# Kernel tuning notes

Measured on AMD Instinct MI355X. Metric: run time of the kernel, lower is better.

## Reference

```python
import jax, jax.numpy as jnp
import numpy as np

N, E, F_IN, H, H2, G, C = 30000, 480000, 1280, 512, 256, 64, 10


def _linear_init(key, fan_in, fan_out):
    k1, k2 = jax.random.split(key)
    s = 1.0 / np.sqrt(fan_in)
    W = jax.random.uniform(k1, (fan_in, fan_out), jnp.float32, -s, s)
    b = jax.random.uniform(k2, (fan_out,), jnp.float32, -s, s)
    return W, b


def setup_inputs() -> dict:
    key = jax.random.key(0)
    ks = jax.random.split(key, 6)
    x = jax.random.normal(ks[0], (N, F_IN), jnp.float32)
    edge_index = jax.random.randint(ks[1], (2, E), 0, N, dtype=jnp.int32).astype(jnp.int64)
    batch = jnp.sort(jax.random.randint(ks[2], (N,), 0, G, dtype=jnp.int32)).astype(jnp.int64)
    W1, b1 = _linear_init(ks[3], F_IN, H)
    beta2 = jnp.ones((), jnp.float32)  # AGNNConv beta init = 1.0 (trainable in prop2)
    W2, b2 = _linear_init(ks[4], H, H2)
    W3, b3 = _linear_init(ks[5], 2 * H2, C)
    return {"x": x, "edge_index": edge_index, "batch": batch,
            "W1": W1, "b1": b1, "beta2": beta2,
            "W2": W2, "b2": b2, "W3": W3, "b3": b3}


def _agnn(x, src, dst, beta, n):
    # L2 normalize (PyG F.normalize: clamp norm at 1e-12)
    norm = jnp.maximum(jnp.linalg.norm(x, axis=-1, keepdims=True), 1e-12)
    xn = x / norm
    # per-edge cosine similarity attention logits
    alpha = beta * jnp.sum(xn[src] * xn[dst], axis=-1)  # [E']
    # softmax over incoming edges of each destination node
    amax = jax.ops.segment_max(alpha, dst, num_segments=n)
    ex = jnp.exp(alpha - amax[dst])
    denom = jax.ops.segment_sum(ex, dst, num_segments=n)
    w = ex / denom[dst]
    # weighted scatter-add of raw source features
    return jax.ops.segment_sum(w[:, None] * x[src], dst, num_segments=n)


def reference(x, edge_index, batch, W1, b1, beta2, W2, b2, W3, b3):
    n = x.shape[0]
    h = jax.nn.relu(x @ W1 + b1)  # [N, 512]
    # AGNNConv adds self-loops by default
    loops = jnp.arange(n, dtype=edge_index.dtype)
    src = jnp.concatenate([edge_index[0], loops])
    dst = jnp.concatenate([edge_index[1], loops])
    h = _agnn(h, src, dst, jnp.float32(1.0), n)  # prop1: fixed beta=1
    h = _agnn(h, src, dst, beta2, n)             # prop2: learned beta
    h = jax.nn.relu(h @ W2 + b2)  # [N, 256]
    # global max / mean pool per graph
    gmx = jax.ops.segment_max(h, batch, num_segments=G)
    cnt = jnp.maximum(jax.ops.segment_sum(jnp.ones((n,), h.dtype), batch, num_segments=G), 1.0)
    gav = jax.ops.segment_sum(h, batch, num_segments=G) / cnt[:, None]
    return jnp.concatenate([gmx, gav], axis=1) @ W3 + b3  # [G, C]
```

## Files before the change

kernel.cpp:

```cpp
#include <hip/hip_runtime.h>
#include <hip/hip_bf16.h>
#include <cstdint>


typedef __attribute__((ext_vector_type(8))) short bf16x8;
typedef __attribute__((ext_vector_type(4))) float f32x4;
typedef __attribute__((ext_vector_type(8))) unsigned short ushort8;
typedef __attribute__((ext_vector_type(4))) unsigned short ushort4v;
typedef __attribute__((ext_vector_type(4))) unsigned int uint4v;

__device__ inline unsigned short f2bf(float f) {
    unsigned int u = __float_as_uint(f);
    u += 0x7FFFu + ((u >> 16) & 1u);
    return (unsigned short)(u >> 16);
}

__device__ __forceinline__ float bf2f(unsigned short u) {
    return __uint_as_float(((unsigned int)u) << 16);
}

__device__ __forceinline__ unsigned int cvtpk(float lo, float hi) {
    unsigned int r;
    asm("v_cvt_pk_bf16_f32 %0, %1, %2" : "=v"(r) : "v"(lo), "v"(hi));
    return r;
}

__device__ __forceinline__ void gload_lds16(const void* g, void* l) {
    __builtin_amdgcn_global_load_lds(
        (const __attribute__((address_space(1))) void*)g,
        (__attribute__((address_space(3))) void*)l, 16, 0, 0);
}

__global__ __launch_bounds__(256) void k_transpose_bf16(
    const float* __restrict__ W, unsigned short* __restrict__ Wt, int K, int N) {
    __shared__ unsigned short t[32][33];
    int k0 = blockIdx.x * 32, n0 = blockIdx.y * 32;
    int tr = threadIdx.x >> 3;
    int tc = (threadIdx.x & 7) * 4;
    float4 v = *(const float4*)(W + (long)(k0 + tr) * N + n0 + tc);
    t[tr][tc + 0] = f2bf(v.x); t[tr][tc + 1] = f2bf(v.y);
    t[tr][tc + 2] = f2bf(v.z); t[tr][tc + 3] = f2bf(v.w);
    __syncthreads();
    ushort4v o = { t[tc + 0][tr], t[tc + 1][tr], t[tc + 2][tr], t[tc + 3][tr] };
    *(ushort4v*)(Wt + (long)(n0 + tr) * K + k0 + tc) = o;
}

template <int K, int N, int WGPB, bool AF32, bool OUTBF16>
__global__ __launch_bounds__(256, WGPB) void k_gemm_bias_relu(
    const void* __restrict__ Av, const unsigned short* __restrict__ Bt,
    const float* __restrict__ bias, void* __restrict__ Cv, int M) {
    constexpr int NF = N / 32;
    __shared__ unsigned short As[2][64 * 32];
    __shared__ unsigned short Bs[2][N * 32];
    int tid = threadIdx.x;
    int w = tid >> 6, l = tid & 63;
    int wm = w >> 1, wn = w & 1;
    int mBase = blockIdx.x * 64;

    const float* Af = (const float*)Av;
    const unsigned short* Ab = (const unsigned short*)Av;

    int arow = tid >> 2;
    int aslot = (tid & 3) ^ ((arow >> 1) & 3);
    long aRowG = mBase + arow; if (aRowG >= M) aRowG = M - 1;
    const float* aptr = AF32 ? (Af + aRowG * K + (tid & 3) * 8) : nullptr;

    auto stageB = [&](int b, int k0) {
#pragma unroll
        for (int o = 0; o < N / 64; ++o) {
            int rbase = (o * 4 + w) * 16;
            int row = rbase + (l >> 2);
            int gsrc = (l & 3) ^ ((row >> 1) & 3);
            gload_lds16(Bt + (long)row * K + k0 + gsrc * 8, &Bs[b][rbase * 32]);
        }
    };
    auto stageAbf = [&](int b, int k0) {
        int rbase = w * 16;
        int row = rbase + (l >> 2);
        int gsrc = (l & 3) ^ ((row >> 1) & 3);
        long gr = mBase + row; if (gr >= M) gr = M - 1;
        gload_lds16(Ab + gr * K + k0 + gsrc * 8, &As[b][rbase * 32]);
    };

    f32x4 acc[2][NF] = {};
    constexpr int NSTEP = K / 32;

    stageB(0, 0);
    if constexpr (AF32) {
        float4 f0 = *(const float4*)(aptr);
        float4 f1 = *(const float4*)(aptr + 4);
        uint4v p = { cvtpk(f0.x, f0.y), cvtpk(f0.z, f0.w),
                     cvtpk(f1.x, f1.y), cvtpk(f1.z, f1.w) };
        *(uint4v*)(&As[0][arow * 32 + aslot * 8]) = p;
    } else {
        stageAbf(0, 0);
    }
    __syncthreads();

    int s = 0;
    for (int step = 0; step < NSTEP; ++step, s ^= 1) {
        int nk = (step + 1) * 32;
        float4 f0, f1;
        if (nk < K) {
            stageB(s ^ 1, nk);
            if constexpr (AF32) {
                f0 = *(const float4*)(aptr + nk);
                f1 = *(const float4*)(aptr + nk + 4);
            } else {
                stageAbf(s ^ 1, nk);
            }
        }
        bf16x8 af[2];
#pragma unroll
        for (int m = 0; m < 2; ++m) {
            int ra = wm * 32 + m * 16 + (l & 15);
            int g = (l >> 4) ^ ((ra >> 1) & 3);
            af[m] = *(const bf16x8*)(&As[s][ra * 32 + g * 8]);
        }
#pragma unroll
        for (int n = 0; n < NF; ++n) {
            int rb = wn * (N / 2) + n * 16 + (l & 15);
            int g = (l >> 4) ^ ((rb >> 1) & 3);
            bf16x8 bfr = *(const bf16x8*)(&Bs[s][rb * 32 + g * 8]);
#pragma unroll
            for (int m = 0; m < 2; ++m)
                acc[m][n] = __builtin_amdgcn_mfma_f32_16x16x32_bf16(
                    af[m], bfr, acc[m][n], 0, 0, 0);
        }
        if constexpr (AF32) {
            if (nk < K) {
                uint4v p = { cvtpk(f0.x, f0.y), cvtpk(f0.z, f0.w),
                             cvtpk(f1.x, f1.y), cvtpk(f1.z, f1.w) };
                *(uint4v*)(&As[s ^ 1][arow * 32 + aslot * 8]) = p;
            }
        }
        __syncthreads();
    }

#pragma unroll
    for (int m = 0; m < 2; ++m) {
        int row = mBase + wm * 32 + m * 16 + (l >> 4) * 4;
#pragma unroll
        for (int n = 0; n < NF; ++n) {
            int colg = wn * (N / 2) + n * 16 + (l & 15);
            float bv = bias[colg];
#pragma unroll
            for (int r = 0; r < 4; ++r) {
                if (row + r < M) {
                    float v = fmaxf(acc[m][n][r] + bv, 0.f);
                    if constexpr (OUTBF16)
                        ((unsigned short*)Cv)[(long)(row + r) * N + colg] = f2bf(v);
                    else
                        ((float*)Cv)[(long)(row + r) * N + colg] = v;
                }
            }
        }
    }
}

__global__ void k_csr_init(int* __restrict__ cnt, int* __restrict__ fill, int n) {
    int i = blockIdx.x * blockDim.x + threadIdx.x;
    if (i < n) { cnt[i] = 1; fill[i] = 0; }
}

__global__ void k_csr_count(const int* __restrict__ ei, int* __restrict__ cnt, int E) {
    int e = blockIdx.x * blockDim.x + threadIdx.x;
    if (e < E) atomicAdd(&cnt[ei[E + e]], 1);
}

__global__ __launch_bounds__(1024) void k_scan1(const int* __restrict__ cnt,
                                                int* __restrict__ rowp,
                                                int* __restrict__ bsum, int n) {
    __shared__ int wsum[16];
    int b = blockIdx.x, t = threadIdx.x, lane = t & 63, w = t >> 6;
    int i = b * 1024 + t;
    int v = (i < n) ? cnt[i] : 0;
    int x = v;
#pragma unroll
    for (int off = 1; off < 64; off <<= 1) {
        int y = __shfl_up(x, off, 64);
        if (lane >= off) x += y;
    }
    if (lane == 63) wsum[w] = x;
    __syncthreads();
    if (t < 16) {
        int s = wsum[t];
#pragma unroll
        for (int off = 1; off < 16; off <<= 1) {
            int y = __shfl_up(s, off, 64);
            if (t >= off) s += y;
        }
        wsum[t] = s;
    }
    __syncthreads();
    int wo = w ? wsum[w - 1] : 0;
    if (i < n) rowp[i] = wo + x - v;
    if (t == 0) bsum[b] = wsum[15];
}

__global__ __launch_bounds__(64) void k_scan2(int* __restrict__ bsum, int nb) {
    int lane = threadIdx.x;
    int v = (lane < nb) ? bsum[lane] : 0;
    int x = v;
#pragma unroll
    for (int off = 1; off < 64; off <<= 1) {
        int y = __shfl_up(x, off, 64);
        if (lane >= off) x += y;
    }
    int total = __shfl(x, nb - 1, 64);
    if (lane < nb) bsum[lane] = x - v;
    if (lane == 0) bsum[nb] = total;
}

__global__ __launch_bounds__(1024) void k_scan3(const int* __restrict__ bsum,
                                                int* __restrict__ rowp, int n, int nb) {
    int i = blockIdx.x * 1024 + threadIdx.x;
    if (i < n) rowp[i] += bsum[i >> 10];
    else if (i == n) rowp[n] = bsum[nb];
}

__global__ void k_csr_fill(const int* __restrict__ ei, const int* __restrict__ rowp,
                           int* __restrict__ fill, int* __restrict__ col, int E, int n) {
    int idx = blockIdx.x * blockDim.x + threadIdx.x;
    if (idx < E) {
        int d = ei[E + idx];
        int s = ei[idx];
        int pos = atomicAdd(&fill[d], 1);
        col[rowp[d] + pos] = s;
    } else if (idx < E + n) {
        int nd = idx - E;
        int pos = atomicAdd(&fill[nd], 1);
        col[rowp[nd] + pos] = nd;
    }
}

__global__ __launch_bounds__(256) void k_norm_bf16(const unsigned short* __restrict__ h,
                                                   float* __restrict__ invn, int n) {
    int row = blockIdx.x * 4 + (threadIdx.x >> 6);
    int lane = threadIdx.x & 63;
    if (row >= n) return;
    ushort8 v = *(const ushort8*)(h + (long)row * 512 + lane * 8);
    float s = 0.f;
#pragma unroll
    for (int e = 0; e < 8; ++e) { float f = bf2f(v[e]); s += f * f; }
#pragma unroll
    for (int off = 32; off; off >>= 1) s += __shfl_xor(s, off, 64);
    if (lane == 0) invn[row] = 1.f / fmaxf(sqrtf(s), 1e-12f);
}

__global__ __launch_bounds__(256) void k_agnn(
    const unsigned short* __restrict__ h, const float* __restrict__ invn,
    const int* __restrict__ rowp, const int* __restrict__ col,
    const float* __restrict__ beta_ptr, unsigned short* __restrict__ out,
    float* __restrict__ invn_out, int nNodes) {
    int dst = blockIdx.x * 4 + (threadIdx.x >> 6);
    int lane = threadIdx.x & 63;
    if (dst >= nNodes) return;
    float beta = beta_ptr ? beta_ptr[0] : 1.0f;
    ushort8 hdv = *(const ushort8*)(h + (long)dst * 512 + lane * 8);
    float hd[8];
#pragma unroll
    for (int e = 0; e < 8; ++e) hd[e] = bf2f(hdv[e]);
    float coef = beta * invn[dst];
    int s0 = rowp[dst], s1 = rowp[dst + 1];

    float m = -1e30f, ssum = 0.f;
    float acc[8] = {0.f, 0.f, 0.f, 0.f, 0.f, 0.f, 0.f, 0.f};

    for (int base = s0; base < s1; base += 64) {
        int cnt = min(s1 - base, 64);
        int gi = base + lane; if (gi >= s1) gi = s1 - 1;
        int idxl = col[gi];
        float vinl = invn[idxl];
        int src0 = __shfl(idxl, 0, 64);
        ushort8 nxt = *(const ushort8*)(h + (long)src0 * 512 + lane * 8);
        for (int j = 0; j < cnt; ++j) {
            ushort8 cur = nxt;
            if (j + 1 < cnt) {
                int sn = __shfl(idxl, j + 1, 64);
                nxt = *(const ushort8*)(h + (long)sn * 512 + lane * 8);
            }
            float a[8];
#pragma unroll
            for (int e = 0; e < 8; ++e) a[e] = bf2f(cur[e]);
            float p = a[0] * hd[0] + a[1] * hd[1] + a[2] * hd[2] + a[3] * hd[3] +
                      a[4] * hd[4] + a[5] * hd[5] + a[6] * hd[6] + a[7] * hd[7];
#pragma unroll
            for (int off = 32; off; off >>= 1) p += __shfl_xor(p, off, 64);
            float alpha = coef * __shfl(vinl, j, 64) * p;
            if (alpha > m) {
                float sc = __expf(m - alpha);
                ssum *= sc;
#pragma unroll
                for (int e = 0; e < 8; ++e) acc[e] *= sc;
                m = alpha;
            }
            float wgt = __expf(alpha - m);
            ssum += wgt;
#pragma unroll
            for (int e = 0; e < 8; ++e) acc[e] += wgt * a[e];
        }
    }
    float inv_s = 1.f / ssum;
#pragma unroll
    for (int e = 0; e < 8; ++e) acc[e] *= inv_s;

    uint4v o = { cvtpk(acc[0], acc[1]), cvtpk(acc[2], acc[3]),
                 cvtpk(acc[4], acc[5]), cvtpk(acc[6], acc[7]) };
    *(uint4v*)(out + (long)dst * 512 + lane * 8) = o;

    if (invn_out) {
        float s = 0.f;
#pragma unroll
        for (int e = 0; e < 8; ++e) s += acc[e] * acc[e];
#pragma unroll
        for (int off = 32; off; off >>= 1) s += __shfl_xor(s, off, 64);
        if (lane == 0) invn_out[dst] = 1.f / fmaxf(sqrtf(s), 1e-12f);
    }
}

__global__ void k_bounds(const int* __restrict__ batch, int* __restrict__ starts,
                         int n, int G) {
    int g = blockIdx.x * blockDim.x + threadIdx.x;
    if (g > G) return;
    int lo = 0, hi = n;
    while (lo < hi) {
        int mid = (lo + hi) >> 1;
        if (batch[mid] < g) lo = mid + 1; else hi = mid;
    }
    starts[g] = lo;
}

__global__ __launch_bounds__(256) void k_pool(const float* __restrict__ h3,
                                              const int* __restrict__ starts,
                                              float* __restrict__ pooled) {
    int g = blockIdx.x;
    int t = threadIdx.x;
    int s = starts[g], e = starts[g + 1];
    float mx = -3.402823466e38f, sm = 0.f;
    int r = s;
    for (; r + 4 <= e; r += 4) {
        float v0 = h3[(long)(r + 0) * 256 + t];
        float v1 = h3[(long)(r + 1) * 256 + t];
        float v2 = h3[(long)(r + 2) * 256 + t];
        float v3 = h3[(long)(r + 3) * 256 + t];
        mx = fmaxf(mx, fmaxf(fmaxf(v0, v1), fmaxf(v2, v3)));
        sm += (v0 + v1) + (v2 + v3);
    }
    for (; r < e; ++r) {
        float v = h3[(long)r * 256 + t];
        mx = fmaxf(mx, v); sm += v;
    }
    float cnt = fmaxf((float)(e - s), 1.f);
    pooled[g * 512 + t] = mx;
    pooled[g * 512 + 256 + t] = sm / cnt;
}

__global__ __launch_bounds__(64) void k_final(const float* __restrict__ pooled,
                                              const float* __restrict__ W3,
                                              const float* __restrict__ b3,
                                              float* __restrict__ out, int C) {
    int g = blockIdx.x;
    int lane = threadIdx.x;
    for (int c = 0; c < C; c++) {
        float p = 0.f;
        for (int k = lane; k < 512; k += 64) p += pooled[g * 512 + k] * W3[k * C + c];
#pragma unroll
        for (int off = 32; off; off >>= 1) p += __shfl_xor(p, off, 64);
        if (lane == 0) out[g * C + c] = p + b3[c];
    }
}

extern "C" void kernel_launch(void* const* d_in, const int* in_sizes, int n_in,
                              void* d_out, int out_size, void* d_ws, size_t ws_size,
                              hipStream_t stream) {
    const float* x     = (const float*)d_in[0];
    const int*   ei    = (const int*)d_in[1];
    const int*   batch = (const int*)d_in[2];
    const float* W1    = (const float*)d_in[3];
    const float* b1    = (const float*)d_in[4];
    const float* beta2 = (const float*)d_in[5];
    const float* W2    = (const float*)d_in[6];
    const float* b2    = (const float*)d_in[7];
    const float* W3    = (const float*)d_in[8];
    const float* b3    = (const float*)d_in[9];
    float* out = (float*)d_out;

    const int N = in_sizes[2];
    const int E = in_sizes[1] / 2;
    const int F_IN = in_sizes[0] / N;
    const int H = in_sizes[4];
    const int H2 = in_sizes[7];
    const int C = in_sizes[9];
    const int G = out_size / C;

    char* ws = (char*)d_ws;
    unsigned short* H1B = (unsigned short*)(ws + 0);
    unsigned short* HPB = (unsigned short*)(ws + 31000000L);
    unsigned short* H2B = (unsigned short*)(ws + 62000000L);
    float*          H3  = (float*)(ws + 0);
    unsigned short* W1T = (unsigned short*)(ws + 93000000L);
    unsigned short* W2T = (unsigned short*)(ws + 94500000L);
    float* INVN_A = (float*)(ws + 95000000L);
    float* INVN_B = (float*)(ws + 95200000L);
    int*   CNT    = (int*)(ws + 95400000L);
    int*   FILL   = (int*)(ws + 95600000L);
    int*   ROWP   = (int*)(ws + 95800000L);
    int*   COL    = (int*)(ws + 96000000L);
    int*   BSUM   = (int*)(ws + 98100000L);
    int*   START  = (int*)(ws + 98110000L);
    float* POOLED = (float*)(ws + 98120000L);

    { dim3 g1(F_IN / 32, H / 32); k_transpose_bf16<<<g1, 256, 0, stream>>>(W1, W1T, F_IN, H); }
    { dim3 g2(H / 32, H2 / 32);   k_transpose_bf16<<<g2, 256, 0, stream>>>(W2, W2T, H, H2); }

    int nb = (N + 1023) / 1024;
    k_csr_init<<<(N + 255) / 256, 256, 0, stream>>>(CNT, FILL, N);
    k_csr_count<<<(E + 255) / 256, 256, 0, stream>>>(ei, CNT, E);
    k_scan1<<<nb, 1024, 0, stream>>>(CNT, ROWP, BSUM, N);
    k_scan2<<<1, 64, 0, stream>>>(BSUM, nb);
    k_scan3<<<(N + 1 + 1023) / 1024, 1024, 0, stream>>>(BSUM, ROWP, N, nb);
    k_csr_fill<<<(E + N + 255) / 256, 256, 0, stream>>>(ei, ROWP, FILL, COL, E, N);

    k_gemm_bias_relu<1280, 512, 2, true, true>
        <<<(N + 63) / 64, 256, 0, stream>>>(x, W1T, b1, H1B, N);

    k_norm_bf16<<<(N + 3) / 4, 256, 0, stream>>>(H1B, INVN_A, N);
    k_agnn<<<(N + 3) / 4, 256, 0, stream>>>(H1B, INVN_A, ROWP, COL, nullptr, HPB, INVN_B, N);

    k_agnn<<<(N + 3) / 4, 256, 0, stream>>>(HPB, INVN_B, ROWP, COL, beta2, H2B, nullptr, N);

    k_gemm_bias_relu<512, 256, 3, false, false>
        <<<(N + 63) / 64, 256, 0, stream>>>(H2B, W2T, b2, H3, N);

    k_bounds<<<1, 128, 0, stream>>>(batch, START, N, G);
    k_pool<<<G, 256, 0, stream>>>(H3, START, POOLED);
    k_final<<<G, 64, 0, stream>>>(POOLED, W3, b3, out, C);
}
```

Measured before the change: 395.1 us.

## Retile GEMMs to 128x256 blocks and use DPP wave reductions in AGNN

Both bias+ReLU GEMMs move to 512-thread blocks that compute a 128-row by 256-column tile, with a second grid dimension splitting the 512-wide output of the first GEMM. Each wave now holds a 64x64 accumulator, which raises MFMA work per LDS fragment load and improves operand reuse, at the cost of more registers per thread and fewer blocks. Separately, the butterfly `__shfl_xor` wave reductions in the norm and AGNN kernels are replaced by a DPP sequence followed by a readlane, and the index and norm broadcasts now use readlane. This cuts LDS-routed shuffle traffic in the per-edge inner loop.

```diff
diff --git a/kernel.cpp b/kernel.cpp
--- a/kernel.cpp
+++ b/kernel.cpp
@@ -29,6 +29,23 @@
     __builtin_amdgcn_global_load_lds(
         (const __attribute__((address_space(1))) void*)g,
         (__attribute__((address_space(3))) void*)l, 16, 0, 0);
+}
+
+__device__ __forceinline__ float wave_sum_dpp(float p) {
+    int t;
+    t = __builtin_amdgcn_update_dpp(0, __float_as_int(p), 0xB1, 0xf, 0xf, true);
+    p += __int_as_float(t);
+    t = __builtin_amdgcn_update_dpp(0, __float_as_int(p), 0x4E, 0xf, 0xf, true);
+    p += __int_as_float(t);
+    t = __builtin_amdgcn_update_dpp(0, __float_as_int(p), 0x141, 0xf, 0xf, true);
+    p += __int_as_float(t);
+    t = __builtin_amdgcn_update_dpp(0, __float_as_int(p), 0x140, 0xf, 0xf, true);
+    p += __int_as_float(t);
+    t = __builtin_amdgcn_update_dpp(0, __float_as_int(p), 0x142, 0xf, 0xf, true);
+    p += __int_as_float(t);
+    t = __builtin_amdgcn_update_dpp(0, __float_as_int(p), 0x143, 0xf, 0xf, true);
+    p += __int_as_float(t);
+    return __int_as_float(__builtin_amdgcn_readlane(__float_as_int(p), 63));
 }
 
 __global__ __launch_bounds__(256) void k_transpose_bf16(
@@ -45,17 +62,17 @@
     *(ushort4v*)(Wt + (long)(n0 + tr) * K + k0 + tc) = o;
 }
 
-template <int K, int N, int WGPB, bool AF32, bool OUTBF16>
-__global__ __launch_bounds__(256, WGPB) void k_gemm_bias_relu(
+template <int K, int BN, int NOUT, bool AF32, bool OUTBF16>
+__global__ __launch_bounds__(512, 4) void k_gemm_bias_relu(
     const void* __restrict__ Av, const unsigned short* __restrict__ Bt,
     const float* __restrict__ bias, void* __restrict__ Cv, int M) {
-    constexpr int NF = N / 32;
-    __shared__ unsigned short As[2][64 * 32];
-    __shared__ unsigned short Bs[2][N * 32];
+    __shared__ unsigned short As[2][128 * 32];
+    __shared__ unsigned short Bs[2][BN * 32];
     int tid = threadIdx.x;
     int w = tid >> 6, l = tid & 63;
-    int wm = w >> 1, wn = w & 1;
-    int mBase = blockIdx.x * 64;
+    int wm = w >> 2, wn = w & 3;
+    int mBase = blockIdx.x * 128;
+    int nBase = blockIdx.y * BN;
 
     const float* Af = (const float*)Av;
     const unsigned short* Ab = (const unsigned short*)Av;
@@ -67,11 +84,12 @@
 
     auto stageB = [&](int b, int k0) {
 #pragma unroll
-        for (int o = 0; o < N / 64; ++o) {
-            int rbase = (o * 4 + w) * 16;
+        for (int o = 0; o < BN / 128; ++o) {
+            int rbase = (w * (BN / 128) + o) * 16;
             int row = rbase + (l >> 2);
             int gsrc = (l & 3) ^ ((row >> 1) & 3);
-            gload_lds16(Bt + (long)row * K + k0 + gsrc * 8, &Bs[b][rbase * 32]);
+            gload_lds16(Bt + (long)(nBase + row) * K + k0 + gsrc * 8,
+                        &Bs[b][rbase * 32]);
         }
     };
     auto stageAbf = [&](int b, int k0) {
@@ -82,7 +100,7 @@
         gload_lds16(Ab + gr * K + k0 + gsrc * 8, &As[b][rbase * 32]);
     };
 
-    f32x4 acc[2][NF] = {};
+    f32x4 acc[4][4] = {};
     constexpr int NSTEP = K / 32;
 
     stageB(0, 0);
@@ -110,20 +128,20 @@
                 stageAbf(s ^ 1, nk);
             }
         }
-        bf16x8 af[2];
-#pragma unroll
-        for (int m = 0; m < 2; ++m) {
-            int ra = wm * 32 + m * 16 + (l & 15);
+        bf16x8 af[4];
+#pragma unroll
+        for (int m = 0; m < 4; ++m) {
+            int ra = wm * 64 + m * 16 + (l & 15);
             int g = (l >> 4) ^ ((ra >> 1) & 3);
             af[m] = *(const bf16x8*)(&As[s][ra * 32 + g * 8]);
         }
 #pragma unroll
-        for (int n = 0; n < NF; ++n) {
-            int rb = wn * (N / 2) + n * 16 + (l & 15);
+        for (int n = 0; n < 4; ++n) {
+            int rb = wn * 64 + n * 16 + (l & 15);
             int g = (l >> 4) ^ ((rb >> 1) & 3);
             bf16x8 bfr = *(const bf16x8*)(&Bs[s][rb * 32 + g * 8]);
 #pragma unroll
-            for (int m = 0; m < 2; ++m)
+            for (int m = 0; m < 4; ++m)
                 acc[m][n] = __builtin_amdgcn_mfma_f32_16x16x32_bf16(
                     af[m], bfr, acc[m][n], 0, 0, 0);
         }
@@ -138,20 +156,20 @@
     }
 
 #pragma unroll
-    for (int m = 0; m < 2; ++m) {
-        int row = mBase + wm * 32 + m * 16 + (l >> 4) * 4;
-#pragma unroll
-        for (int n = 0; n < NF; ++n) {
-            int colg = wn * (N / 2) + n * 16 + (l & 15);
+    for (int m = 0; m < 4; ++m) {
+        int row = mBase + wm * 64 + m * 16 + (l >> 4) * 4;
+#pragma unroll
+        for (int n = 0; n < 4; ++n) {
+            int colg = nBase + wn * 64 + n * 16 + (l & 15);
             float bv = bias[colg];
 #pragma unroll
             for (int r = 0; r < 4; ++r) {
                 if (row + r < M) {
                     float v = fmaxf(acc[m][n][r] + bv, 0.f);
                     if constexpr (OUTBF16)
-                        ((unsigned short*)Cv)[(long)(row + r) * N + colg] = f2bf(v);
+                        ((unsigned short*)Cv)[(long)(row + r) * NOUT + colg] = f2bf(v);
                     else
-                        ((float*)Cv)[(long)(row + r) * N + colg] = v;
+                        ((float*)Cv)[(long)(row + r) * NOUT + colg] = v;
                 }
             }
         }
@@ -243,8 +261,7 @@
     float s = 0.f;
 #pragma unroll
     for (int e = 0; e < 8; ++e) { float f = bf2f(v[e]); s += f * f; }
-#pragma unroll
-    for (int off = 32; off; off >>= 1) s += __shfl_xor(s, off, 64);
+    s = wave_sum_dpp(s);
     if (lane == 0) invn[row] = 1.f / fmaxf(sqrtf(s), 1e-12f);
 }
 
@@ -272,12 +289,12 @@
         int gi = base + lane; if (gi >= s1) gi = s1 - 1;
         int idxl = col[gi];
         float vinl = invn[idxl];
-        int src0 = __shfl(idxl, 0, 64);
+        int src0 = __builtin_amdgcn_readlane(idxl, 0);
         ushort8 nxt = *(const ushort8*)(h + (long)src0 * 512 + lane * 8);
         for (int j = 0; j < cnt; ++j) {
             ushort8 cur = nxt;
             if (j + 1 < cnt) {
-                int sn = __shfl(idxl, j + 1, 64);
+                int sn = __builtin_amdgcn_readlane(idxl, j + 1);
                 nxt = *(const ushort8*)(h + (long)sn * 512 + lane * 8);
             }
             float a[8];
@@ -285,9 +302,10 @@
             for (int e = 0; e < 8; ++e) a[e] = bf2f(cur[e]);
             float p = a[0] * hd[0] + a[1] * hd[1] + a[2] * hd[2] + a[3] * hd[3] +
                       a[4] * hd[4] + a[5] * hd[5] + a[6] * hd[6] + a[7] * hd[7];
-#pragma unroll
-            for (int off = 32; off; off >>= 1) p += __shfl_xor(p, off, 64);
-            float alpha = coef * __shfl(vinl, j, 64) * p;
+            p = wave_sum_dpp(p);
+            float vin_j = __int_as_float(
+                __builtin_amdgcn_readlane(__float_as_int(vinl), j));
+            float alpha = coef * vin_j * p;
             if (alpha > m) {
                 float sc = __expf(m - alpha);
                 ssum *= sc;
@@ -313,8 +331,7 @@
         float s = 0.f;
 #pragma unroll
         for (int e = 0; e < 8; ++e) s += acc[e] * acc[e];
-#pragma unroll
-        for (int off = 32; off; off >>= 1) s += __shfl_xor(s, off, 64);
+        s = wave_sum_dpp(s);
         if (lane == 0) invn_out[dst] = 1.f / fmaxf(sqrtf(s), 1e-12f);
     }
 }
@@ -422,16 +439,22 @@
     k_scan3<<<(N + 1 + 1023) / 1024, 1024, 0, stream>>>(BSUM, ROWP, N, nb);
     k_csr_fill<<<(E + N + 255) / 256, 256, 0, stream>>>(ei, ROWP, FILL, COL, E, N);
 
-    k_gemm_bias_relu<1280, 512, 2, true, true>
-        <<<(N + 63) / 64, 256, 0, stream>>>(x, W1T, b1, H1B, N);
+    {
+        dim3 grid((N + 127) / 128, H / 256);
+        k_gemm_bias_relu<1280, 256, 512, true, true>
+            <<<grid, 512, 0, stream>>>(x, W1T, b1, H1B, N);
+    }
 
     k_norm_bf16<<<(N + 3) / 4, 256, 0, stream>>>(H1B, INVN_A, N);
     k_agnn<<<(N + 3) / 4, 256, 0, stream>>>(H1B, INVN_A, ROWP, COL, nullptr, HPB, INVN_B, N);
 
     k_agnn<<<(N + 3) / 4, 256, 0, stream>>>(HPB, INVN_B, ROWP, COL, beta2, H2B, nullptr, N);
 
-    k_gemm_bias_relu<512, 256, 3, false, false>
-        <<<(N + 63) / 64, 256, 0, stream>>>(H2B, W2T, b2, H3, N);
+    {
+        dim3 grid((N + 127) / 128, 1);
+        k_gemm_bias_relu<512, 256, 256, false, false>
+            <<<grid, 512, 0, stream>>>(H2B, W2T, b2, H3, N);
+    }
 
     k_bounds<<<1, 128, 0, stream>>>(batch, START, N, G);
     k_pool<<<G, 256, 0, stream>>>(H3, START, POOLED);
```

Measured after the change: 376.2 us. -4.8%, faster.
